# Kernel optimization log

Hardware: AMD Instinct MI355X
Metric: run time of the kernel (lower is better)

## Reference

```python
import jax, jax.numpy as jnp
import numpy as np

H = 16          # num_heads
LN_EPS = 1e-5


def _layernorm(x, g, b):
    mu = jnp.mean(x, axis=-1, keepdims=True)
    var = jnp.mean(jnp.square(x - mu), axis=-1, keepdims=True)
    return (x - mu) * jax.lax.rsqrt(var + LN_EPS) * g + b


def setup_inputs() -> dict:
    key = jax.random.key(0)
    ks = jax.random.split(key, 4)
    B, T, D = 32, 1024, 1024
    s = 1.0 / np.sqrt(D)
    return {
        "x": jax.random.normal(ks[0], (B, T, D), dtype=jnp.float32),
        "ln_g": jnp.ones((D,), jnp.float32),
        "ln_b": jnp.zeros((D,), jnp.float32),
        "Wq": jax.random.normal(ks[1], (D, D), dtype=jnp.float32) * s,
        "bq": jnp.zeros((D,), jnp.float32),
        "Wk": jax.random.normal(ks[2], (D, D), dtype=jnp.float32) * s,
        "bk": jnp.zeros((D,), jnp.float32),
        "Wv": jax.random.normal(ks[3], (D, D), dtype=jnp.float32) * s,
        "bv": jnp.zeros((D,), jnp.float32),
    }


def reference(x, ln_g, ln_b, Wq, bq, Wk, bk, Wv, bv):
    B, T, D = x.shape
    d = D // H
    xn = _layernorm(x, ln_g, ln_b)                       # [B,T,D]
    # torch Linear: y = x @ W.T + b, W is [out, in]
    q = jnp.einsum('btd,ed->bte', xn, Wq) + bq
    k = jnp.einsum('btd,ed->bte', xn, Wk) + bk
    v = (jnp.einsum('btd,ed->bte', xn, Wv) + bv).reshape(B, T, H, d)
    q = jax.nn.softmax(q.reshape(B, T, H, d), axis=-1)   # softmax over head dim
    k = jax.nn.softmax(k.reshape(B, T, H, d), axis=1)    # softmax over sequence
    # linear attention: context [B,H,d,d], then project queries through it
    attn = jnp.einsum('bnhd,bnhl->bhdl', k, v)
    y = jnp.einsum('bnhd,bhdl->bnhl', q, attn).reshape(B, T, D)
    return x + y
```

## Files before the change

kernel.cpp:

```cpp
#include <hip/hip_runtime.h>
#include <stdint.h>

typedef __attribute__((ext_vector_type(4))) float  f32x4;
typedef __attribute__((ext_vector_type(8))) short  short8;
typedef __attribute__((ext_vector_type(4))) short  short4v;
typedef __attribute__((ext_vector_type(2))) unsigned int uint2v;

#define DEV __device__ __forceinline__

DEV float b2f(unsigned short u) { return __uint_as_float(((unsigned)u) << 16); }
DEV unsigned short f2b(float f) {
  unsigned u = __float_as_uint(f);
  return (unsigned short)((u + 0x7fffu + ((u >> 16) & 1u)) >> 16);
}

#define AS1C(p) ((const __attribute__((address_space(1))) void*)(uintptr_t)(p))
#define AS3(p)  ((__attribute__((address_space(3))) void*)(unsigned)(uintptr_t)(p))
DEV void gload16(const void* g, void* l) {
  __builtin_amdgcn_global_load_lds(AS1C(g), AS3(l), 16, 0, 0);
}

static constexpr int B_ = 32, T_ = 1024, D_ = 1024;
static constexpr int M_ = B_ * T_;
static constexpr int N3 = 3 * D_;

__global__ __launch_bounds__(256) void cvt_weights(
    const float* __restrict__ Wq, const float* __restrict__ Wk, const float* __restrict__ Wv,
    const float* __restrict__ bq, const float* __restrict__ bk, const float* __restrict__ bv,
    unsigned short* __restrict__ Wcat, float* __restrict__ bias,
    float* __restrict__ ksum)
{
  int idx = blockIdx.x * 256 + threadIdx.x;
  int which = idx >> 18;
  int rem   = idx & 262143;
  const float* src = which == 0 ? Wq : (which == 1 ? Wk : Wv);
  f32x4 v = reinterpret_cast<const f32x4*>(src)[rem];
  uint2v p;
  p[0] = (unsigned)f2b(v[0]) | ((unsigned)f2b(v[1]) << 16);
  p[1] = (unsigned)f2b(v[2]) | ((unsigned)f2b(v[3]) << 16);
  reinterpret_cast<uint2v*>(Wcat)[idx] = p;
  if (idx < 3072) {
    const float* bsrc = idx < 1024 ? bq : (idx < 2048 ? bk : bv);
    bias[idx] = bsrc[idx & 1023];
  }
  if (idx < 32768) ksum[idx] = 0.f;
}

__global__ __launch_bounds__(256) void ln_kernel(
    const float* __restrict__ x, const float* __restrict__ g, const float* __restrict__ b,
    unsigned short* __restrict__ xn)
{
  int row = blockIdx.x;
  int tid = threadIdx.x;
  const f32x4 v = reinterpret_cast<const f32x4*>(x + (size_t)row * D_)[tid];
  float s  = v[0] + v[1] + v[2] + v[3];
  float s2 = v[0]*v[0] + v[1]*v[1] + v[2]*v[2] + v[3]*v[3];
  #pragma unroll
  for (int o = 32; o > 0; o >>= 1) { s += __shfl_down(s, o); s2 += __shfl_down(s2, o); }
  __shared__ float rs_[4], rs2_[4];
  int lane = tid & 63, wave = tid >> 6;
  if (lane == 0) { rs_[wave] = s; rs2_[wave] = s2; }
  __syncthreads();
  float S  = rs_[0] + rs_[1] + rs_[2] + rs_[3];
  float S2 = rs2_[0] + rs2_[1] + rs2_[2] + rs2_[3];
  float mu = S * (1.f / D_);
  float var = S2 * (1.f / D_) - mu * mu;
  float rstd = rsqrtf(var + 1e-5f);
  const f32x4 gg = reinterpret_cast<const f32x4*>(g)[tid];
  const f32x4 bb = reinterpret_cast<const f32x4*>(b)[tid];
  float y0 = (v[0]-mu)*rstd*gg[0] + bb[0];
  float y1 = (v[1]-mu)*rstd*gg[1] + bb[1];
  float y2 = (v[2]-mu)*rstd*gg[2] + bb[2];
  float y3 = (v[3]-mu)*rstd*gg[3] + bb[3];
  uint2v p;
  p[0] = (unsigned)f2b(y0) | ((unsigned)f2b(y1) << 16);
  p[1] = (unsigned)f2b(y2) | ((unsigned)f2b(y3) << 16);
  reinterpret_cast<uint2v*>(xn + (size_t)row * D_)[tid] = p;
}

__global__ __launch_bounds__(512, 2) void gemm_qkv(
    const unsigned short* __restrict__ A,
    const unsigned short* __restrict__ Bm,
    const float* __restrict__ bias,
    unsigned short* __restrict__ C,
    float* __restrict__ ksum)
{
  __shared__ alignas(16) short lds[4 * 16384];
  const int tid = threadIdx.x;
  constexpr int nbn = N3 / 256;
  constexpr int nwg = (M_ / 256) * nbn;
  int wg = blockIdx.x;
  int swzb = (wg & 7) * (nwg >> 3) + (wg >> 3);
  int bm = swzb / nbn, bn = swzb % nbn;
  int arow = bm * 256, bcol = bn * 256;
  int lane = tid & 63, wave = tid >> 6;
  int wr = wave >> 2, wc = wave & 3;
  int g = lane >> 4, r = lane & 15;

  const unsigned short* Ab = A  + (size_t)arow * 1024;
  const unsigned short* Bb = Bm + (size_t)bcol * 1024;

  int rho = (wave << 4) | (lane >> 2);
  int pg  = (lane & 3) ^ ((rho >> 1) & 3);
  size_t gR0 = (size_t)rho * 1024 + pg * 8;
  size_t gR1 = (size_t)(rho + 128) * 1024 + pg * 8;
  int lofs = wave * 512;

  #define STAGE_A(t) { short* bb0 = lds + (((t) & 3) << 14); int k2 = (t) << 5; \
    gload16(Ab + k2 + gR0, (void*)(bb0 + lofs)); \
    gload16(Ab + k2 + gR1, (void*)(bb0 + 4096 + lofs)); }
  #define STAGE_B(t) { short* bb0 = lds + (((t) & 3) << 14); int k2 = (t) << 5; \
    gload16(Bb + k2 + gR0, (void*)(bb0 + 8192 + lofs)); \
    gload16(Bb + k2 + gR1, (void*)(bb0 + 12288 + lofs)); }

  f32x4 acc[8][4] = {};
  STAGE_A(0); STAGE_B(0);
  STAGE_A(1); STAGE_B(1);
  STAGE_A(2); STAGE_B(2);
  asm volatile("s_waitcnt vmcnt(8)" ::: "memory");
  __builtin_amdgcn_s_barrier();

  for (int t = 0; t < 32; ++t) {
    const short* bufA = lds + ((t & 3) << 14);
    const short* bufB = bufA + 8192;
    short8 a[8], bfr[4];
    #pragma unroll
    for (int mi = 0; mi < 8; ++mi) {
      int row = wr * 128 + mi * 16 + r;
      a[mi] = *(const short8*)(bufA + row * 32 + ((g ^ ((row >> 1) & 3)) << 3));
    }
    #pragma unroll
    for (int ni = 0; ni < 4; ++ni) {
      int row = wc * 64 + ni * 16 + r;
      bfr[ni] = *(const short8*)(bufB + row * 32 + ((g ^ ((row >> 1) & 3)) << 3));
    }
    if (t < 29) { STAGE_A(t + 3); STAGE_B(t + 3); }
    __builtin_amdgcn_s_setprio(1);
    #pragma unroll
    for (int mi = 0; mi < 8; ++mi)
      #pragma unroll
      for (int ni = 0; ni < 4; ++ni)
        acc[mi][ni] = __builtin_amdgcn_mfma_f32_16x16x32_bf16(a[mi], bfr[ni], acc[mi][ni], 0, 0, 0);
    __builtin_amdgcn_s_setprio(0);
    if (t < 29)       { asm volatile("s_waitcnt vmcnt(8)" ::: "memory"); }
    else if (t == 29) { asm volatile("s_waitcnt vmcnt(4)" ::: "memory"); }
    else if (t == 30) { asm volatile("s_waitcnt vmcnt(0)" ::: "memory"); }
    __builtin_amdgcn_s_barrier();
  }
  #undef STAGE_A
  #undef STAGE_B

  float bs[4];
  #pragma unroll
  for (int ni = 0; ni < 4; ++ni) bs[ni] = bias[bcol + wc * 64 + ni * 16 + r];
  bool isK = (bcol >= 1024 && bcol < 2048);
  if (isK) {
    float ks[4] = {0.f, 0.f, 0.f, 0.f};
    #pragma unroll
    for (int mi = 0; mi < 8; ++mi)
      #pragma unroll
      for (int j = 0; j < 4; ++j) {
        int rowl = wr * 128 + mi * 16 + 4 * g + j;
        size_t rb = (size_t)(arow + rowl) * N3 + bcol + wc * 64 + r;
        #pragma unroll
        for (int ni = 0; ni < 4; ++ni) {
          unsigned short cv = f2b(acc[mi][ni][j] + bs[ni]);
          C[rb + ni * 16] = cv;
          ks[ni] += __expf(b2f(cv));
        }
      }
    int b = arow >> 10;
    #pragma unroll
    for (int ni = 0; ni < 4; ++ni) {
      float s = ks[ni];
      s += __shfl_xor(s, 16);
      s += __shfl_xor(s, 32);
      if (g == 0)
        atomicAdd(&ksum[b * 1024 + (bcol - 1024) + wc * 64 + ni * 16 + r], s);
    }
  } else {
    #pragma unroll
    for (int mi = 0; mi < 8; ++mi)
      #pragma unroll
      for (int j = 0; j < 4; ++j) {
        int rowl = wr * 128 + mi * 16 + 4 * g + j;
        size_t rb = (size_t)(arow + rowl) * N3 + bcol + wc * 64 + r;
        #pragma unroll
        for (int ni = 0; ni < 4; ++ni)
          C[rb + ni * 16] = f2b(acc[mi][ni][j] + bs[ni]);
      }
  }
}

__global__ __launch_bounds__(256) void attn_kernel(
    const unsigned short* __restrict__ qkv, const float* __restrict__ ksum,
    float* __restrict__ attnP)
{
  int bid = blockIdx.x;
  int bh = bid >> 2, tq = bid & 3;
  int b = bh >> 4, h = bh & 15;
  int tid = threadIdx.x;
  int cgrp = tid & 7, trow = tid >> 3;
  int lane = tid & 63, wave = tid >> 6;
  int g = lane >> 4, r = lane & 15;
  __shared__ alignas(16) short lK[64 * 40];
  __shared__ alignas(16) short lV[64 * 40];
  const unsigned short* kb = qkv + ((size_t)(b * T_ + tq * 256)) * N3 + D_     + h * 64;
  const unsigned short* vb = qkv + ((size_t)(b * T_ + tq * 256)) * N3 + 2 * D_ + h * 64;
  float inv[8];
  const float* kp = ksum + b * 1024 + h * 64 + cgrp * 8;
  #pragma unroll
  for (int j = 0; j < 8; ++j) inv[j] = 1.f / kp[j];
  f32x4 acc[4] = {};
  short8 kv = *(const short8*)(kb + (size_t)trow * N3 + cgrp * 8);
  short8 vv = *(const short8*)(vb + (size_t)trow * N3 + cgrp * 8);
  for (int tc = 0; tc < 8; ++tc) {
    __syncthreads();
    #pragma unroll
    for (int j = 0; j < 8; ++j) {
      lK[(cgrp * 8 + j) * 40 + trow] =
          (short)f2b(__expf(b2f((unsigned short)kv[j])) * inv[j]);
      lV[(cgrp * 8 + j) * 40 + trow] = vv[j];
    }
    __syncthreads();
    if (tc < 7) {
      kv = *(const short8*)(kb + (size_t)((tc + 1) * 32 + trow) * N3 + cgrp * 8);
      vv = *(const short8*)(vb + (size_t)((tc + 1) * 32 + trow) * N3 + cgrp * 8);
    }
    short8 af = *(const short8*)(lK + (16 * wave + r) * 40 + 8 * g);
    #pragma unroll
    for (int ni = 0; ni < 4; ++ni) {
      short8 bf = *(const short8*)(lV + (16 * ni + r) * 40 + 8 * g);
      acc[ni] = __builtin_amdgcn_mfma_f32_16x16x32_bf16(af, bf, acc[ni], 0, 0, 0);
    }
  }
  float* op = attnP + (size_t)bid * 4096;
  #pragma unroll
  for (int ni = 0; ni < 4; ++ni)
    #pragma unroll
    for (int j = 0; j < 4; ++j) {
      int m = 16 * wave + 4 * g + j;
      int n = 16 * ni + r;
      op[(size_t)n * 64 + m] = acc[ni][j];
    }
}

__global__ __launch_bounds__(256) void attn_reduce(
    const float* __restrict__ attnP, unsigned short* __restrict__ attnT)
{
  int bh = blockIdx.x;
  int tid = threadIdx.x;
  const float* p0 = attnP + ((size_t)bh << 2) * 4096;
  unsigned short* o = attnT + (size_t)bh * 4096;
  #pragma unroll
  for (int it = 0; it < 4; ++it) {
    int i = (it * 256 + tid) * 4;
    f32x4 s  = *(const f32x4*)(p0 + i);
    f32x4 s1 = *(const f32x4*)(p0 + 4096 + i);
    f32x4 s2 = *(const f32x4*)(p0 + 8192 + i);
    f32x4 s3 = *(const f32x4*)(p0 + 12288 + i);
    s[0] += s1[0] + s2[0] + s3[0];
    s[1] += s1[1] + s2[1] + s3[1];
    s[2] += s1[2] + s2[2] + s3[2];
    s[3] += s1[3] + s2[3] + s3[3];
    short4v ov;
    ov[0] = (short)f2b(s[0]); ov[1] = (short)f2b(s[1]);
    ov[2] = (short)f2b(s[2]); ov[3] = (short)f2b(s[3]);
    *(short4v*)(o + i) = ov;
  }
}

__global__ __launch_bounds__(256) void out_kernel(
    const unsigned short* __restrict__ qkv, const unsigned short* __restrict__ attnT,
    const float* __restrict__ x, float* __restrict__ out)
{
  int bid = blockIdx.x;
  int bh = bid >> 3, mt = bid & 7;
  int b = bh >> 4, h = bh & 15;
  int tid = threadIdx.x;
  int lane = tid & 63, wave = tid >> 6;
  int g = lane >> 4, r = lane & 15;
  __shared__ alignas(16) short lAT[64 * 72];
  __shared__ float lO[128][66];
  const unsigned short* at = attnT + (size_t)bh * 4096;
  #pragma unroll
  for (int i = 0; i < 2; ++i) {
    int idx8 = (i * 256 + tid) * 8;
    int n = idx8 >> 6, kk0 = idx8 & 63;
    *(short8*)(lAT + n * 72 + kk0) = *(const short8*)(at + idx8);
  }
  __syncthreads();
  short8 bt[4][2];
  #pragma unroll
  for (int ni = 0; ni < 4; ++ni)
    #pragma unroll
    for (int kc = 0; kc < 2; ++kc)
      bt[ni][kc] = *(const short8*)(lAT + (16 * ni + r) * 72 + kc * 32 + 8 * g);
  int rowbase = mt * 128 + 32 * wave;
  const unsigned short* qb = qkv + (size_t)(b * T_ + rowbase) * N3 + h * 64;
  short8 aq[2][2];
  #pragma unroll
  for (int mi = 0; mi < 2; ++mi) {
    float qe[16];
    float s = 0.f;
    #pragma unroll
    for (int kc = 0; kc < 2; ++kc) {
      short8 qa = *(const short8*)(qb + (size_t)(16 * mi + r) * N3 + kc * 32 + 8 * g);
      #pragma unroll
      for (int j = 0; j < 8; ++j) {
        float e = __expf(b2f((unsigned short)qa[j]));
        qe[kc * 8 + j] = e;
        s += e;
      }
    }
    s += __shfl_xor(s, 16);
    s += __shfl_xor(s, 32);
    float inv = 1.f / s;
    #pragma unroll
    for (int kc = 0; kc < 2; ++kc) {
      short8 t8;
      #pragma unroll
      for (int j = 0; j < 8; ++j) t8[j] = (short)f2b(qe[kc * 8 + j] * inv);
      aq[mi][kc] = t8;
    }
  }
  f32x4 acc[2][4] = {};
  #pragma unroll
  for (int mi = 0; mi < 2; ++mi)
    #pragma unroll
    for (int kc = 0; kc < 2; ++kc)
      #pragma unroll
      for (int ni = 0; ni < 4; ++ni)
        acc[mi][ni] = __builtin_amdgcn_mfma_f32_16x16x32_bf16(aq[mi][kc], bt[ni][kc], acc[mi][ni], 0, 0, 0);
  #pragma unroll
  for (int mi = 0; mi < 2; ++mi)
    #pragma unroll
    for (int ni = 0; ni < 4; ++ni)
      #pragma unroll
      for (int j = 0; j < 4; ++j)
        lO[32 * wave + 16 * mi + 4 * g + j][16 * ni + r] = acc[mi][ni][j];
  __syncthreads();
  int rr = tid >> 4, c4 = (tid & 15) << 2;
  #pragma unroll
  for (int p = 0; p < 8; ++p) {
    int rowl = p * 16 + rr;
    size_t gi = ((size_t)(b * T_ + mt * 128 + rowl) << 10) + h * 64 + c4;
    f32x4 xv = *(const f32x4*)(x + gi);
    f32x4 ov;
    ov[0] = xv[0] + lO[rowl][c4];
    ov[1] = xv[1] + lO[rowl][c4 + 1];
    ov[2] = xv[2] + lO[rowl][c4 + 2];
    ov[3] = xv[3] + lO[rowl][c4 + 3];
    *(f32x4*)(out + gi) = ov;
  }
}

extern "C" void kernel_launch(void* const* d_in, const int* in_sizes, int n_in,
                              void* d_out, int out_size, void* d_ws, size_t ws_size,
                              hipStream_t stream) {
  const float* x   = (const float*)d_in[0];
  const float* lng = (const float*)d_in[1];
  const float* lnb = (const float*)d_in[2];
  const float* Wq  = (const float*)d_in[3];
  const float* bq  = (const float*)d_in[4];
  const float* Wk  = (const float*)d_in[5];
  const float* bk  = (const float*)d_in[6];
  const float* Wv  = (const float*)d_in[7];
  const float* bv  = (const float*)d_in[8];
  float* out = (float*)d_out;
  char* ws = (char*)d_ws;
  unsigned short* Wcat  = (unsigned short*)(ws + 0);
  float*          bias  = (float*)         (ws + 6291456);
  unsigned short* xn    = (unsigned short*)(ws + 6303744);
  unsigned short* qkv   = (unsigned short*)(ws + 73412608);
  unsigned short* attnT = (unsigned short*)(ws + 274739200);
  float* attnP = (float*)xn;
  float* ksum = (float*)d_out;
  cvt_weights<<<3072,  256, 0, stream>>>(Wq, Wk, Wv, bq, bk, bv, Wcat, bias, ksum);
  ln_kernel  <<<M_,    256, 0, stream>>>(x, lng, lnb, xn);
  gemm_qkv   <<<1536,  512, 0, stream>>>(xn, Wcat, bias, qkv, ksum);
  attn_kernel<<<2048,  256, 0, stream>>>(qkv, ksum, attnP);
  attn_reduce<<<512,   256, 0, stream>>>(attnP, attnT);
  out_kernel <<<4096,  256, 0, stream>>>(qkv, attnT, x, out);
}
```

Before: 376.6 us.

## Merge weight conversion with layernorm, store attention partials as bf16, prefetch residual

```diff
diff --git a/kernel.cpp b/kernel.cpp
--- a/kernel.cpp
+++ b/kernel.cpp
@@ -24,34 +24,33 @@
 static constexpr int M_ = B_ * T_;
 static constexpr int N3 = 3 * D_;
 
-__global__ __launch_bounds__(256) void cvt_weights(
+__global__ __launch_bounds__(256) void prep_kernel(
     const float* __restrict__ Wq, const float* __restrict__ Wk, const float* __restrict__ Wv,
     const float* __restrict__ bq, const float* __restrict__ bk, const float* __restrict__ bv,
+    const float* __restrict__ x, const float* __restrict__ lng, const float* __restrict__ lnb,
     unsigned short* __restrict__ Wcat, float* __restrict__ bias,
-    float* __restrict__ ksum)
-{
-  int idx = blockIdx.x * 256 + threadIdx.x;
-  int which = idx >> 18;
-  int rem   = idx & 262143;
-  const float* src = which == 0 ? Wq : (which == 1 ? Wk : Wv);
-  f32x4 v = reinterpret_cast<const f32x4*>(src)[rem];
-  uint2v p;
-  p[0] = (unsigned)f2b(v[0]) | ((unsigned)f2b(v[1]) << 16);
-  p[1] = (unsigned)f2b(v[2]) | ((unsigned)f2b(v[3]) << 16);
-  reinterpret_cast<uint2v*>(Wcat)[idx] = p;
-  if (idx < 3072) {
-    const float* bsrc = idx < 1024 ? bq : (idx < 2048 ? bk : bv);
-    bias[idx] = bsrc[idx & 1023];
-  }
-  if (idx < 32768) ksum[idx] = 0.f;
-}
-
-__global__ __launch_bounds__(256) void ln_kernel(
-    const float* __restrict__ x, const float* __restrict__ g, const float* __restrict__ b,
-    unsigned short* __restrict__ xn)
-{
-  int row = blockIdx.x;
+    float* __restrict__ ksum, unsigned short* __restrict__ xn)
+{
+  int bid = blockIdx.x;
   int tid = threadIdx.x;
+  if (bid < 3072) {
+    int idx = bid * 256 + tid;
+    int which = idx >> 18;
+    int rem   = idx & 262143;
+    const float* src = which == 0 ? Wq : (which == 1 ? Wk : Wv);
+    f32x4 v = reinterpret_cast<const f32x4*>(src)[rem];
+    uint2v p;
+    p[0] = (unsigned)f2b(v[0]) | ((unsigned)f2b(v[1]) << 16);
+    p[1] = (unsigned)f2b(v[2]) | ((unsigned)f2b(v[3]) << 16);
+    reinterpret_cast<uint2v*>(Wcat)[idx] = p;
+    if (idx < 3072) {
+      const float* bsrc = idx < 1024 ? bq : (idx < 2048 ? bk : bv);
+      bias[idx] = bsrc[idx & 1023];
+    }
+    if (idx < 32768) ksum[idx] = 0.f;
+    return;
+  }
+  int row = bid - 3072;
   const f32x4 v = reinterpret_cast<const f32x4*>(x + (size_t)row * D_)[tid];
   float s  = v[0] + v[1] + v[2] + v[3];
   float s2 = v[0]*v[0] + v[1]*v[1] + v[2]*v[2] + v[3]*v[3];
@@ -66,8 +65,8 @@
   float mu = S * (1.f / D_);
   float var = S2 * (1.f / D_) - mu * mu;
   float rstd = rsqrtf(var + 1e-5f);
-  const f32x4 gg = reinterpret_cast<const f32x4*>(g)[tid];
-  const f32x4 bb = reinterpret_cast<const f32x4*>(b)[tid];
+  const f32x4 gg = reinterpret_cast<const f32x4*>(lng)[tid];
+  const f32x4 bb = reinterpret_cast<const f32x4*>(lnb)[tid];
   float y0 = (v[0]-mu)*rstd*gg[0] + bb[0];
   float y1 = (v[1]-mu)*rstd*gg[1] + bb[1];
   float y2 = (v[2]-mu)*rstd*gg[2] + bb[2];
@@ -194,7 +193,7 @@
 
 __global__ __launch_bounds__(256) void attn_kernel(
     const unsigned short* __restrict__ qkv, const float* __restrict__ ksum,
-    float* __restrict__ attnP)
+    unsigned short* __restrict__ attnP)
 {
   int bid = blockIdx.x;
   int bh = bid >> 2, tq = bid & 3;
@@ -234,39 +233,39 @@
       acc[ni] = __builtin_amdgcn_mfma_f32_16x16x32_bf16(af, bf, acc[ni], 0, 0, 0);
     }
   }
-  float* op = attnP + (size_t)bid * 4096;
+  unsigned short* op = attnP + (size_t)bid * 4096;
   #pragma unroll
   for (int ni = 0; ni < 4; ++ni)
     #pragma unroll
     for (int j = 0; j < 4; ++j) {
       int m = 16 * wave + 4 * g + j;
       int n = 16 * ni + r;
-      op[(size_t)n * 64 + m] = acc[ni][j];
+      op[(size_t)n * 64 + m] = f2b(acc[ni][j]);
     }
 }
 
 __global__ __launch_bounds__(256) void attn_reduce(
-    const float* __restrict__ attnP, unsigned short* __restrict__ attnT)
+    const unsigned short* __restrict__ attnP, unsigned short* __restrict__ attnT)
 {
   int bh = blockIdx.x;
   int tid = threadIdx.x;
-  const float* p0 = attnP + ((size_t)bh << 2) * 4096;
+  const unsigned short* p0 = attnP + ((size_t)bh << 2) * 4096;
   unsigned short* o = attnT + (size_t)bh * 4096;
   #pragma unroll
-  for (int it = 0; it < 4; ++it) {
-    int i = (it * 256 + tid) * 4;
-    f32x4 s  = *(const f32x4*)(p0 + i);
-    f32x4 s1 = *(const f32x4*)(p0 + 4096 + i);
-    f32x4 s2 = *(const f32x4*)(p0 + 8192 + i);
-    f32x4 s3 = *(const f32x4*)(p0 + 12288 + i);
-    s[0] += s1[0] + s2[0] + s3[0];
-    s[1] += s1[1] + s2[1] + s3[1];
-    s[2] += s1[2] + s2[2] + s3[2];
-    s[3] += s1[3] + s2[3] + s3[3];
-    short4v ov;
-    ov[0] = (short)f2b(s[0]); ov[1] = (short)f2b(s[1]);
-    ov[2] = (short)f2b(s[2]); ov[3] = (short)f2b(s[3]);
-    *(short4v*)(o + i) = ov;
+  for (int it = 0; it < 2; ++it) {
+    int i = (it * 256 + tid) * 8;
+    short8 s0 = *(const short8*)(p0 + i);
+    short8 s1 = *(const short8*)(p0 + 4096 + i);
+    short8 s2 = *(const short8*)(p0 + 8192 + i);
+    short8 s3 = *(const short8*)(p0 + 12288 + i);
+    short8 ov;
+    #pragma unroll
+    for (int j = 0; j < 8; ++j) {
+      float s = b2f((unsigned short)s0[j]) + b2f((unsigned short)s1[j])
+              + b2f((unsigned short)s2[j]) + b2f((unsigned short)s3[j]);
+      ov[j] = (short)f2b(s);
+    }
+    *(short8*)(o + i) = ov;
   }
 }
 
@@ -282,6 +281,14 @@
   int g = lane >> 4, r = lane & 15;
   __shared__ alignas(16) short lAT[64 * 72];
   __shared__ float lO[128][66];
+  int rr = tid >> 4, c4 = (tid & 15) << 2;
+  f32x4 xv[8];
+  #pragma unroll
+  for (int p = 0; p < 8; ++p) {
+    int rowl = p * 16 + rr;
+    size_t gi = ((size_t)(b * T_ + mt * 128 + rowl) << 10) + h * 64 + c4;
+    xv[p] = *(const f32x4*)(x + gi);
+  }
   const unsigned short* at = attnT + (size_t)bh * 4096;
   #pragma unroll
   for (int i = 0; i < 2; ++i) {
@@ -340,17 +347,15 @@
       for (int j = 0; j < 4; ++j)
         lO[32 * wave + 16 * mi + 4 * g + j][16 * ni + r] = acc[mi][ni][j];
   __syncthreads();
-  int rr = tid >> 4, c4 = (tid & 15) << 2;
   #pragma unroll
   for (int p = 0; p < 8; ++p) {
     int rowl = p * 16 + rr;
     size_t gi = ((size_t)(b * T_ + mt * 128 + rowl) << 10) + h * 64 + c4;
-    f32x4 xv = *(const f32x4*)(x + gi);
     f32x4 ov;
-    ov[0] = xv[0] + lO[rowl][c4];
-    ov[1] = xv[1] + lO[rowl][c4 + 1];
-    ov[2] = xv[2] + lO[rowl][c4 + 2];
-    ov[3] = xv[3] + lO[rowl][c4 + 3];
+    ov[0] = xv[p][0] + lO[rowl][c4];
+    ov[1] = xv[p][1] + lO[rowl][c4 + 1];
+    ov[2] = xv[p][2] + lO[rowl][c4 + 2];
+    ov[3] = xv[p][3] + lO[rowl][c4 + 3];
     *(f32x4*)(out + gi) = ov;
   }
 }
@@ -374,10 +379,10 @@
   unsigned short* xn    = (unsigned short*)(ws + 6303744);
   unsigned short* qkv   = (unsigned short*)(ws + 73412608);
   unsigned short* attnT = (unsigned short*)(ws + 274739200);
-  float* attnP = (float*)xn;
+  unsigned short* attnP = (unsigned short*)xn;
   float* ksum = (float*)d_out;
-  cvt_weights<<<3072,  256, 0, stream>>>(Wq, Wk, Wv, bq, bk, bv, Wcat, bias, ksum);
-  ln_kernel  <<<M_,    256, 0, stream>>>(x, lng, lnb, xn);
+  prep_kernel<<<3072 + M_, 256, 0, stream>>>(Wq, Wk, Wv, bq, bk, bv,
+                                             x, lng, lnb, Wcat, bias, ksum, xn);
   gemm_qkv   <<<1536,  512, 0, stream>>>(xn, Wcat, bias, qkv, ksum);
   attn_kernel<<<2048,  256, 0, stream>>>(qkv, ksum, attnP);
   attn_reduce<<<512,   256, 0, stream>>>(attnP, attnT);
```

Measured after the change: 374.9 us (median of 2 runs). About the same (-0.4%).
